# Kernel optimization log

Hardware: AMD Instinct MI355X
Metric: run time of the kernel (lower is better)

## Reference

```python
import jax, jax.numpy as jnp
import numpy as np
import math

B, S, D, H = 4, 2048, 1024, 16
HD = D // H

def setup_inputs() -> dict:
    key = jax.random.key(0)
    ks = jax.random.split(key, 14)
    scale = 1.0 / math.sqrt(D)
    inp = {
        "q": jax.random.normal(ks[0], (B, S, D), jnp.float32),
        "k": jax.random.normal(ks[1], (B, S, D), jnp.float32),
        "v": jax.random.normal(ks[2], (B, S, D), jnp.float32),
        "time_diffs": jax.random.uniform(ks[3], (B, S, S), jnp.float32),
        "mask": jax.random.randint(ks[4], (B, 1, S, S), 0, 2, jnp.int32),
        "Wq": jax.random.normal(ks[5], (D, D), jnp.float32) * scale,
        "bq": jnp.zeros((D,), jnp.float32),
        "Wk": jax.random.normal(ks[6], (D, D), jnp.float32) * scale,
        "bk": jnp.zeros((D,), jnp.float32),
        "Wv": jax.random.normal(ks[7], (D, D), jnp.float32) * scale,
        "bv": jnp.zeros((D,), jnp.float32),
        "Wo": jax.random.normal(ks[8], (D, D), jnp.float32) * scale,
        "bo": jnp.zeros((D,), jnp.float32),
        "gamma": jnp.asarray(1.0, jnp.float32),
    }
    return inp


def reference(q, k, v, time_diffs, mask, Wq, bq, Wk, bk, Wv, bv, Wo, bo, gamma):
    # Linear projections (torch Linear: x @ W.T + b), split heads -> [B,H,S,HD]
    def proj(x, W, b):
        return (x @ W.T + b).reshape(B, S, H, HD).transpose(0, 2, 1, 3)

    qh = proj(q, Wq, bq)
    kh = proj(k, Wk, bk)
    vh = proj(v, Wv, bv)

    # [B,H,S,S] attention scores
    scores = jnp.einsum("bhqd,bhkd->bhqk", qh, kh) / math.sqrt(HD)
    # additive time-decay bias, broadcast over heads
    scores = scores + jnp.exp(-gamma * time_diffs)[:, None, :, :]
    scores = jnp.where(mask == 0, jnp.float32(-1e9), scores)

    attn = jax.nn.softmax(scores, axis=-1)
    # dropout is identity in eval mode (training=False)
    out = jnp.einsum("bhqk,bhkd->bhqd", attn, vh)
    out = out.transpose(0, 2, 1, 3).reshape(B, S, D)
    return out @ Wo.T + bo
```

## Files before the change

### kernel.cpp

```cpp
#include <hip/hip_runtime.h>
#include <hip/hip_bf16.h>

#define B_ 4
#define S_ 2048
#define D_ 1024
#define H_ 16
#define M_ 8192

typedef __attribute__((ext_vector_type(8))) _Float16 h8;
typedef __attribute__((ext_vector_type(4))) _Float16 h4;
typedef __attribute__((ext_vector_type(2))) __fp16   fp16x2;
typedef __attribute__((ext_vector_type(8))) short    s8;
typedef __attribute__((ext_vector_type(4))) float    f4;

#define AS1(p) ((const __attribute__((address_space(1))) void*)(p))
#define AS3(p) ((__attribute__((address_space(3))) void*)(p))

__device__ __forceinline__ f4 mfma16(h8 a, h8 b, f4 c) {
  return __builtin_amdgcn_mfma_f32_16x16x32_f16(a, b, c, 0, 0, 0);
}

struct CastArgs {
  const float* src[7];
  _Float16*    dst[7];
  int cum[8];
};

__global__ __launch_bounds__(256) void cast_kernel(CastArgs a) {
  int idx = blockIdx.x * 256 + threadIdx.x;
  if (idx >= a.cum[7]) return;
  int seg = 0;
#pragma unroll
  for (int s = 1; s < 7; ++s) seg += (idx >= a.cum[s]) ? 1 : 0;
  size_t off = (size_t)(idx - a.cum[seg]) * 8;
  const float4* sp = (const float4*)(a.src[seg] + off);
  float4 u = sp[0], v = sp[1];
  union { _Float16 h[8]; h8 v8; } o;
  o.h[0] = (_Float16)u.x; o.h[1] = (_Float16)u.y;
  o.h[2] = (_Float16)u.z; o.h[3] = (_Float16)u.w;
  o.h[4] = (_Float16)v.x; o.h[5] = (_Float16)v.y;
  o.h[6] = (_Float16)v.z; o.h[7] = (_Float16)v.w;
  *(h8*)(a.dst[seg] + off) = o.v8;
}

__global__ __launch_bounds__(256) void bias_kernel(
    const float* __restrict__ td, const int* __restrict__ mask,
    const float* __restrict__ gptr, _Float16* __restrict__ biasN)
{
  const float gamma = gptr[0];
  size_t idx = (size_t)blockIdx.x * 256 + threadIdx.x;
  size_t off = idx * 8;
  const float4* tp = (const float4*)(td + off);
  const int4*   mp = (const int4*)(mask + off);
  float4 t0 = tp[0], t1 = tp[1];
  int4   m0 = mp[0], m1 = mp[1];
  union { _Float16 h[8]; h8 v8; } o;
  o.h[0] = m0.x ? (_Float16)(__expf(-gamma * t0.x) * 1.4426950408889634f) : (_Float16)(-30000.0f);
  o.h[1] = m0.y ? (_Float16)(__expf(-gamma * t0.y) * 1.4426950408889634f) : (_Float16)(-30000.0f);
  o.h[2] = m0.z ? (_Float16)(__expf(-gamma * t0.z) * 1.4426950408889634f) : (_Float16)(-30000.0f);
  o.h[3] = m0.w ? (_Float16)(__expf(-gamma * t0.w) * 1.4426950408889634f) : (_Float16)(-30000.0f);
  o.h[4] = m1.x ? (_Float16)(__expf(-gamma * t1.x) * 1.4426950408889634f) : (_Float16)(-30000.0f);
  o.h[5] = m1.y ? (_Float16)(__expf(-gamma * t1.y) * 1.4426950408889634f) : (_Float16)(-30000.0f);
  o.h[6] = m1.z ? (_Float16)(__expf(-gamma * t1.z) * 1.4426950408889634f) : (_Float16)(-30000.0f);
  o.h[7] = m1.w ? (_Float16)(__expf(-gamma * t1.w) * 1.4426950408889634f) : (_Float16)(-30000.0f);
  *(h8*)(biasN + off) = o.v8;
}

template<bool F32OUT>
__global__ __launch_bounds__(256, 3) void gemm_bt(
    const _Float16* __restrict__ A,
    const _Float16* __restrict__ Bt,
    const float*    __restrict__ bias,
    void*           __restrict__ Cout,
    float scale)
{
  __shared__ __align__(16) _Float16 Alds[128 * 64];
  __shared__ __align__(16) _Float16 Blds[128 * 64];
  const int t = threadIdx.x;
  const int lane = t & 63, w = t >> 6;
  const int wm = w >> 1, wn = w & 1;
  const int m0 = blockIdx.x * 128, n0 = blockIdx.y * 128;
  const int ll = lane & 15, lg = lane >> 4;
  f4 acc[4][4] = {};

  for (int kt = 0; kt < 1024; kt += 64) {
    __syncthreads();
#pragma unroll
    for (int i = 0; i < 4; ++i) {
      int slot = i * 256 + t;
      int r = slot >> 3;
      int gs = ((slot & 7) ^ (r & 7)) * 8;
      __builtin_amdgcn_global_load_lds(AS1(A  + (size_t)(m0 + r) * 1024 + kt + gs),
                                       AS3((char*)Alds + (i * 256 + w * 64) * 16), 16, 0, 0);
      __builtin_amdgcn_global_load_lds(AS1(Bt + (size_t)(n0 + r) * 1024 + kt + gs),
                                       AS3((char*)Blds + (i * 256 + w * 64) * 16), 16, 0, 0);
    }
    __syncthreads();
#pragma unroll
    for (int ks = 0; ks < 2; ++ks) {
      h8 af[4], bf[4];
#pragma unroll
      for (int im = 0; im < 4; ++im) {
        int R = wm * 64 + im * 16 + ll;
        af[im] = *(const h8*)((const char*)Alds + R * 128 + (((ks * 4 + lg) ^ (R & 7)) << 4));
      }
#pragma unroll
      for (int in = 0; in < 4; ++in) {
        int R = wn * 64 + in * 16 + ll;
        bf[in] = *(const h8*)((const char*)Blds + R * 128 + (((ks * 4 + lg) ^ (R & 7)) << 4));
      }
#pragma unroll
      for (int im = 0; im < 4; ++im)
#pragma unroll
        for (int in = 0; in < 4; ++in)
          acc[im][in] = mfma16(af[im], bf[in], acc[im][in]);
    }
  }
#pragma unroll
  for (int im = 0; im < 4; ++im)
#pragma unroll
    for (int in = 0; in < 4; ++in) {
      int col = n0 + wn * 64 + in * 16 + ll;
      float bv = bias[col];
#pragma unroll
      for (int r = 0; r < 4; ++r) {
        int row = m0 + wm * 64 + im * 16 + lg * 4 + r;
        float vv = (acc[im][in][r] + bv) * scale;
        if constexpr (F32OUT) ((float*)Cout)[(size_t)row * 1024 + col] = vv;
        else ((_Float16*)Cout)[(size_t)row * 1024 + col] = (_Float16)vv;
      }
    }
}

__global__ __launch_bounds__(256) void transpose_v(
    const _Float16* __restrict__ Vp, _Float16* __restrict__ Vt)
{
  __shared__ __align__(16) short tile[64][72];
  const int blk = blockIdx.x;
  const int b = blk >> 9, h = (blk >> 5) & 15, st = blk & 31;
  const int s0 = st * 64, t = threadIdx.x;
#pragma unroll
  for (int it = 0; it < 2; ++it) {
    int slot = it * 256 + t;
    int r = slot >> 3, c = slot & 7;
    s8 v = *(const s8*)(Vp + (size_t)(b * S_ + s0 + r) * D_ + h * 64 + c * 8);
    *(s8*)&tile[r][c * 8] = v;
  }
  __syncthreads();
#pragma unroll
  for (int it = 0; it < 2; ++it) {
    int slot = it * 256 + t;
    int hd = slot >> 3, c = slot & 7;
    union { short hh[8]; s8 v8; } o;
#pragma unroll
    for (int e = 0; e < 8; ++e) o.hh[e] = tile[c * 8 + e][hd];
    *(s8*)(Vt + (size_t)((b * 16 + h) * 64 + hd) * S_ + s0 + c * 8) = o.v8;
  }
}

#define KL_OFF   0
#define VL_OFF   16384
#define PL_OFF   32768

__global__ __launch_bounds__(256, 4) void attn_kernel(
    const _Float16* __restrict__ Qp,
    const _Float16* __restrict__ Kp,
    const _Float16* __restrict__ Vt,
    const _Float16* __restrict__ biasN,
    _Float16*       __restrict__ Oa)
{
  __shared__ __align__(16) char lds[40960];
  const int t = threadIdx.x;
  const int lane = t & 63, w = t >> 6;
  const int ll = lane & 15, lg = lane >> 4;
  const int bid = blockIdx.x;
  const int b  = bid >> 9;
  const int h  = (bid >> 5) & 15;
  const int qg = bid & 31;
  const int q0 = qg * 64 + w * 16;

  const int lrow = lane >> 3;
  const int lcs  = (lane & 7) ^ lrow;

  const _Float16* Kg = Kp + (size_t)b * S_ * D_ + h * 64;
  const _Float16* Vg = Vt + (size_t)(b * 16 + h) * 64 * S_;
  const _Float16* Bg = biasN + ((size_t)b * S_ + q0 + ll) * S_;

  char* pbase = lds + PL_OFF + w * 2048;

  const size_t qrow = (size_t)(b * S_ + q0 + ll) * D_ + h * 64;
  h8 qf0 = *(const h8*)(Qp + qrow + lg * 8);
  h8 qf1 = *(const h8*)(Qp + qrow + 32 + lg * 8);

  float lsum = 0.f;
  f4 accO[4] = {};

  auto STAGE = [&](int kt, int bufb) {
#pragma unroll
    for (int j = 0; j < 4; ++j) {
      int i = w * 4 + j;
      int g = i & 7;
      int row8 = g * 8 + lrow;
      const _Float16* src;
      char* dst;
      if (i < 8) {
        src = Kg + (size_t)(kt + row8) * D_ + lcs * 8;
        dst = lds + KL_OFF + bufb * 8192 + g * 1024;
      } else {
        src = Vg + (size_t)row8 * S_ + kt + lcs * 8;
        dst = lds + VL_OFF + bufb * 8192 + g * 1024;
      }
      __builtin_amdgcn_global_load_lds(AS1(src), AS3(dst), 16, 0, 0);
    }
  };
  auto BLOAD = [&](int kt, h4 (&dst)[4]) {
#pragma unroll
    for (int jf = 0; jf < 4; ++jf)
      dst[jf] = *(const h4*)(Bg + kt + 16 * jf + lg * 4);
  };

  auto BODY = [&](int tt, h4 (&bc)[4], h4 (&bn)[4]) {
    const int bufb = tt & 1;
    const char* Kb = lds + KL_OFF + bufb * 8192;
    const char* Vb = lds + VL_OFF + bufb * 8192;

    f4 accS[4];
#pragma unroll
    for (int jf = 0; jf < 4; ++jf) {
      accS[jf][0] = (float)bc[jf][0];
      accS[jf][1] = (float)bc[jf][1];
      accS[jf][2] = (float)bc[jf][2];
      accS[jf][3] = (float)bc[jf][3];
    }
#pragma unroll
    for (int jf = 0; jf < 4; ++jf) {
      int row = jf * 16 + ll;
      h8 k0 = *(const h8*)(Kb + row * 128 + (((lg)     ^ (row & 7)) << 4));
      h8 k1 = *(const h8*)(Kb + row * 128 + (((4 + lg) ^ (row & 7)) << 4));
      accS[jf] = mfma16(k0, qf0, accS[jf]);
      accS[jf] = mfma16(k1, qf1, accS[jf]);
    }

    if (tt < 31) {
      STAGE((tt + 1) * 64, bufb ^ 1);
      BLOAD((tt + 1) * 64, bn);
    }

#pragma unroll
    for (int jf = 0; jf < 4; ++jf) {
      float p0, p1, p2, p3;
      asm("v_exp_f32 %0, %1" : "=v"(p0) : "v"(accS[jf][0]));
      asm("v_exp_f32 %0, %1" : "=v"(p1) : "v"(accS[jf][1]));
      asm("v_exp_f32 %0, %1" : "=v"(p2) : "v"(accS[jf][2]));
      asm("v_exp_f32 %0, %1" : "=v"(p3) : "v"(accS[jf][3]));
      lsum += (p0 + p1) + (p2 + p3);
      union { fp16x2 h[2]; unsigned long long u; } wv;
      wv.h[0] = __builtin_amdgcn_cvt_pkrtz(p0, p1);
      wv.h[1] = __builtin_amdgcn_cvt_pkrtz(p2, p3);
      *(unsigned long long*)(pbase + ll * 128 + ((32 * jf + 8 * lg) ^ ((ll & 7) << 4))) = wv.u;
    }

#pragma unroll
    for (int ks = 0; ks < 2; ++ks) {
      h8 pf = *(const h8*)(pbase + ll * 128 + ((ks * 64 + lg * 16) ^ ((ll & 7) << 4)));
#pragma unroll
      for (int df = 0; df < 4; ++df) {
        int vrow = df * 16 + ll;
        h8 vfr = *(const h8*)(Vb + vrow * 128 + (((ks * 4 + lg) ^ (vrow & 7)) << 4));
        accO[df] = mfma16(vfr, pf, accO[df]);
      }
    }

    __syncthreads();
  };

  h4 bA[4], bB[4];

  STAGE(0, 0);
  BLOAD(0, bA);
  __syncthreads();

  for (int tt = 0; tt < 32; tt += 2) {
    BODY(tt,     bA, bB);
    BODY(tt + 1, bB, bA);
  }

  lsum += __shfl_xor(lsum, 16);
  lsum += __shfl_xor(lsum, 32);
  float linv = 1.0f / lsum;
#pragma unroll
  for (int df = 0; df < 4; ++df)
#pragma unroll
    for (int r = 0; r < 4; ++r) {
      size_t orow = (size_t)(b * S_ + q0 + ll) * D_ + h * 64 + df * 16 + lg * 4 + r;
      Oa[orow] = (_Float16)(accO[df][r] * linv);
    }
}

extern "C" void kernel_launch(void* const* d_in, const int* in_sizes, int n_in,
                              void* d_out, int out_size, void* d_ws, size_t ws_size,
                              hipStream_t stream) {
  const float* q    = (const float*)d_in[0];
  const float* k    = (const float*)d_in[1];
  const float* v    = (const float*)d_in[2];
  const float* td   = (const float*)d_in[3];
  const int*   mask = (const int*)d_in[4];
  const float* Wq   = (const float*)d_in[5];
  const float* bq   = (const float*)d_in[6];
  const float* Wk   = (const float*)d_in[7];
  const float* bk   = (const float*)d_in[8];
  const float* Wv   = (const float*)d_in[9];
  const float* bv   = (const float*)d_in[10];
  const float* Wo   = (const float*)d_in[11];
  const float* bo   = (const float*)d_in[12];
  const float* gm   = (const float*)d_in[13];

  const size_t MD = (size_t)M_ * D_;
  const size_t WW = (size_t)D_ * D_;
  if (ws_size < (8 * MD + 4 * WW) * sizeof(_Float16)) return;

  _Float16* base = (_Float16*)d_ws;
  _Float16* qh = base;
  _Float16* kh = qh + MD;
  _Float16* vh = kh + MD;
  _Float16* wq = vh + MD;
  _Float16* wk = wq + WW;
  _Float16* wv = wk + WW;
  _Float16* wo = wv + WW;
  _Float16* Qp = wo + WW;
  _Float16* Kp = Qp + MD;
  _Float16* Vp = Kp + MD;
  _Float16* Vt = Vp + MD;
  _Float16* Oa = Vt + MD;
  _Float16* biasN = qh;

  CastArgs ca;
  ca.src[0] = q;  ca.src[1] = k;  ca.src[2] = v;
  ca.src[3] = Wq; ca.src[4] = Wk; ca.src[5] = Wv; ca.src[6] = Wo;
  ca.dst[0] = qh; ca.dst[1] = kh; ca.dst[2] = vh;
  ca.dst[3] = wq; ca.dst[4] = wk; ca.dst[5] = wv; ca.dst[6] = wo;
  int sizes[7] = {(int)(MD / 8), (int)(MD / 8), (int)(MD / 8),
                  (int)(WW / 8), (int)(WW / 8), (int)(WW / 8), (int)(WW / 8)};
  int c = 0; ca.cum[0] = 0;
  for (int i = 0; i < 7; ++i) { c += sizes[i]; ca.cum[i + 1] = c; }
  cast_kernel<<<(c + 255) / 256, 256, 0, stream>>>(ca);

  dim3 gg(64, 8);
  gemm_bt<false><<<gg, 256, 0, stream>>>(qh, wq, bq, Qp, 0.18033688011112042f);
  gemm_bt<false><<<gg, 256, 0, stream>>>(kh, wk, bk, Kp, 1.0f);
  bias_kernel<<<8192, 256, 0, stream>>>(td, mask, gm, biasN);
  gemm_bt<false><<<gg, 256, 0, stream>>>(vh, wv, bv, Vp, 1.0f);
  transpose_v<<<2048, 256, 0, stream>>>(Vp, Vt);
  attn_kernel<<<2048, 256, 0, stream>>>(Qp, Kp, Vt, biasN, Oa);
  gemm_bt<true><<<gg, 256, 0, stream>>>(Oa, wo, bo, d_out, 1.0f);
}
```

Measured before the change: 325.3 us.

## Fuse V transpose into V projection epilogue and remap attention block order

The V projection GEMM now writes its output directly in the transposed per-head layout with packed 4-element stores, so the separate transpose_v kernel and its extra round trip through memory are removed. The attention kernel also remaps blockIdx so that consecutive blocks land in different XCD groups (stride-8 interleave), which should improve L2 locality for the K/V of each head. The trade-off is that the transposed stores are scattered 8-byte writes instead of coalesced rows.

```diff
diff --git a/kernel.cpp b/kernel.cpp
--- a/kernel.cpp
+++ b/kernel.cpp
@@ -66,7 +66,7 @@
   *(h8*)(biasN + off) = o.v8;
 }
 
-template<bool F32OUT>
+template<int MODE>
 __global__ __launch_bounds__(256, 3) void gemm_bt(
     const _Float16* __restrict__ A,
     const _Float16* __restrict__ Bt,
@@ -122,40 +122,25 @@
     for (int in = 0; in < 4; ++in) {
       int col = n0 + wn * 64 + in * 16 + ll;
       float bv = bias[col];
-#pragma unroll
-      for (int r = 0; r < 4; ++r) {
-        int row = m0 + wm * 64 + im * 16 + lg * 4 + r;
-        float vv = (acc[im][in][r] + bv) * scale;
-        if constexpr (F32OUT) ((float*)Cout)[(size_t)row * 1024 + col] = vv;
-        else ((_Float16*)Cout)[(size_t)row * 1024 + col] = (_Float16)vv;
-      }
-    }
-}
-
-__global__ __launch_bounds__(256) void transpose_v(
-    const _Float16* __restrict__ Vp, _Float16* __restrict__ Vt)
-{
-  __shared__ __align__(16) short tile[64][72];
-  const int blk = blockIdx.x;
-  const int b = blk >> 9, h = (blk >> 5) & 15, st = blk & 31;
-  const int s0 = st * 64, t = threadIdx.x;
-#pragma unroll
-  for (int it = 0; it < 2; ++it) {
-    int slot = it * 256 + t;
-    int r = slot >> 3, c = slot & 7;
-    s8 v = *(const s8*)(Vp + (size_t)(b * S_ + s0 + r) * D_ + h * 64 + c * 8);
-    *(s8*)&tile[r][c * 8] = v;
-  }
-  __syncthreads();
-#pragma unroll
-  for (int it = 0; it < 2; ++it) {
-    int slot = it * 256 + t;
-    int hd = slot >> 3, c = slot & 7;
-    union { short hh[8]; s8 v8; } o;
-#pragma unroll
-    for (int e = 0; e < 8; ++e) o.hh[e] = tile[c * 8 + e][hd];
-    *(s8*)(Vt + (size_t)((b * 16 + h) * 64 + hd) * S_ + s0 + c * 8) = o.v8;
-  }
+      if constexpr (MODE == 2) {
+        int row0 = m0 + wm * 64 + im * 16 + lg * 4;
+        int bb = row0 >> 11, s = row0 & 2047;
+        union { _Float16 hh[4]; unsigned long long u; } pk;
+#pragma unroll
+        for (int r = 0; r < 4; ++r)
+          pk.hh[r] = (_Float16)((acc[im][in][r] + bv) * scale);
+        _Float16* Vt = (_Float16*)Cout;
+        *(unsigned long long*)(Vt + (size_t)((bb * 16 + (col >> 6)) * 64 + (col & 63)) * S_ + s) = pk.u;
+      } else {
+#pragma unroll
+        for (int r = 0; r < 4; ++r) {
+          int row = m0 + wm * 64 + im * 16 + lg * 4 + r;
+          float vv = (acc[im][in][r] + bv) * scale;
+          if constexpr (MODE == 1) ((float*)Cout)[(size_t)row * 1024 + col] = vv;
+          else ((_Float16*)Cout)[(size_t)row * 1024 + col] = (_Float16)vv;
+        }
+      }
+    }
 }
 
 #define KL_OFF   0
@@ -173,10 +158,10 @@
   const int t = threadIdx.x;
   const int lane = t & 63, w = t >> 6;
   const int ll = lane & 15, lg = lane >> 4;
-  const int bid = blockIdx.x;
-  const int b  = bid >> 9;
-  const int h  = (bid >> 5) & 15;
-  const int qg = bid & 31;
+  const int vbid = ((int)blockIdx.x & 7) * 256 + ((int)blockIdx.x >> 3);
+  const int b  = vbid >> 9;
+  const int h  = (vbid >> 5) & 15;
+  const int qg = vbid & 31;
   const int q0 = qg * 64 + w * 16;
 
   const int lrow = lane >> 3;
@@ -346,11 +331,10 @@
   cast_kernel<<<(c + 255) / 256, 256, 0, stream>>>(ca);
 
   dim3 gg(64, 8);
-  gemm_bt<false><<<gg, 256, 0, stream>>>(qh, wq, bq, Qp, 0.18033688011112042f);
-  gemm_bt<false><<<gg, 256, 0, stream>>>(kh, wk, bk, Kp, 1.0f);
+  gemm_bt<0><<<gg, 256, 0, stream>>>(qh, wq, bq, Qp, 0.18033688011112042f);
+  gemm_bt<0><<<gg, 256, 0, stream>>>(kh, wk, bk, Kp, 1.0f);
   bias_kernel<<<8192, 256, 0, stream>>>(td, mask, gm, biasN);
-  gemm_bt<false><<<gg, 256, 0, stream>>>(vh, wv, bv, Vp, 1.0f);
-  transpose_v<<<2048, 256, 0, stream>>>(Vp, Vt);
+  gemm_bt<2><<<gg, 256, 0, stream>>>(vh, wv, bv, Vt, 1.0f);
   attn_kernel<<<2048, 256, 0, stream>>>(Qp, Kp, Vt, biasN, Oa);
-  gemm_bt<true><<<gg, 256, 0, stream>>>(Oa, wo, bo, d_out, 1.0f);
-}
+  gemm_bt<1><<<gg, 256, 0, stream>>>(Oa, wo, bo, d_out, 1.0f);
+}
```

Result: no change. 320.3 us (-1.5%).
